# Optimization experiments

Hardware: AMD Instinct MI355X
Metric: run time of the kernel (lower is better)

The kernel has to match this reference:

```python
import jax, jax.numpy as jnp
import numpy as np

EPS = 1e-5

def _ln(x, g, b):
    mu = jnp.mean(x, axis=-1, keepdims=True)
    var = jnp.mean((x - mu) ** 2, axis=-1, keepdims=True)
    return (x - mu) * jax.lax.rsqrt(var + EPS) * g + b

def _leaky(x):
    return jax.nn.leaky_relu(x, 0.1)

def _gather(feats, idx):
    # feats: [B,N,C], idx: [B,M,K] -> [B,M,K,C]
    return jax.vmap(lambda f, i: f[i])(feats, idx)

def _forward(dense_xyz, dense_feats, pe_w1, pe_b1, pe_g1, pe_be1, pe_w2, pe_b2, pe_g2, pe_be2,
             wn_w1, wn_b1, wn_g1, wn_be1, wn_w2, wn_b2, wn_g2, wn_be2, wn_w3, wn_b3, wn_g3, wn_be3,
             nm_g, nm_b, l1_w, l1_b, l2_w, l2_b, sc_w, sc_b, nei_inds):
    gathered_xyz = _gather(dense_xyz, nei_inds)             # [B,M,K,3]
    localized = gathered_xyz - dense_xyz[:, :, None, :]     # relative coords (no subsampling: M==N)
    # pe_convs WeightNet: 3 -> 32 -> 32, LayerNorm per layer, LeakyReLU(0.1) except last
    h = _leaky(_ln(localized @ pe_w1 + pe_b1, pe_g1, pe_be1))
    feat_pe = _ln(h @ pe_w2 + pe_b2, pe_g2, pe_be2)         # [B,M,K,32]
    # weightnet: 3 -> 16 -> 16 -> Cin (per-edge depthwise weights)
    w = _leaky(_ln(localized @ wn_w1 + wn_b1, wn_g1, wn_be1))
    w = _leaky(_ln(w @ wn_w2 + wn_b2, wn_g2, wn_be2))
    w = _ln(w @ wn_w3 + wn_b3, wn_g3, wn_be3)               # [B,M,K,Cin]
    gathered_feat = _gather(dense_feats, nei_inds)          # [B,M,K,Cin]
    # depthwise aggregation over K, pe channels aggregated alongside
    agg = jnp.concatenate([jnp.sum(gathered_feat * w, axis=2), jnp.sum(feat_pe, axis=2)], axis=-1)
    x = _ln(agg, nm_g, nm_b)                                # LayerNorm(Cin+32)
    x = _leaky(x @ l1_w + l1_b)                             # inverted bottleneck 288 -> 1024
    x = x @ l2_w + l2_b                                     # 1024 -> Cout
    shortcut = dense_feats @ sc_w + sc_b                    # unary shortcut Cin -> Cout
    return _leaky(shortcut + x)

def setup_inputs():
    key = jax.random.key(0)
    B, N, K, CIN, COUT, PE, H = 1, 32768, 16, 256, 512, 32, 16
    ks = jax.random.split(key, 12)
    def g(k, shape, s=0.02):
        return jax.random.normal(k, shape, dtype=jnp.float32) * s
    return {
        "dense_xyz": jax.random.uniform(ks[0], (B, N, 3), dtype=jnp.float32),
        "dense_feats": jax.random.normal(ks[1], (B, N, CIN), dtype=jnp.float32),
        "nei_inds": jax.random.randint(ks[2], (B, N, K), 0, N),
        "pe_w1": g(ks[3], (3, PE), 0.2), "pe_b1": jnp.zeros((PE,), jnp.float32),
        "pe_g1": jnp.ones((PE,), jnp.float32), "pe_be1": jnp.zeros((PE,), jnp.float32),
        "pe_w2": g(ks[4], (PE, PE), 0.1), "pe_b2": jnp.zeros((PE,), jnp.float32),
        "pe_g2": jnp.ones((PE,), jnp.float32), "pe_be2": jnp.zeros((PE,), jnp.float32),
        "wn_w1": g(ks[5], (3, H), 0.2), "wn_b1": jnp.zeros((H,), jnp.float32),
        "wn_g1": jnp.ones((H,), jnp.float32), "wn_be1": jnp.zeros((H,), jnp.float32),
        "wn_w2": g(ks[6], (H, H), 0.1), "wn_b2": jnp.zeros((H,), jnp.float32),
        "wn_g2": jnp.ones((H,), jnp.float32), "wn_be2": jnp.zeros((H,), jnp.float32),
        "wn_w3": g(ks[7], (H, CIN), 0.1), "wn_b3": jnp.zeros((CIN,), jnp.float32),
        "wn_g3": jnp.ones((CIN,), jnp.float32), "wn_be3": jnp.zeros((CIN,), jnp.float32),
        "nm_g": jnp.ones((CIN + PE,), jnp.float32), "nm_b": jnp.zeros((CIN + PE,), jnp.float32),
        "l1_w": g(ks[8], (CIN + PE, 4 * CIN)), "l1_b": jnp.zeros((4 * CIN,), jnp.float32),
        "l2_w": g(ks[9], (4 * CIN, COUT)), "l2_b": jnp.zeros((COUT,), jnp.float32),
        "sc_w": g(ks[10], (CIN, COUT)), "sc_b": jnp.zeros((COUT,), jnp.float32),
    }

def reference(dense_xyz, dense_feats, nei_inds, pe_w1, pe_b1, pe_g1, pe_be1, pe_w2, pe_b2, pe_g2, pe_be2,
              wn_w1, wn_b1, wn_g1, wn_be1, wn_w2, wn_b2, wn_g2, wn_be2, wn_w3, wn_b3, wn_g3, wn_be3,
              nm_g, nm_b, l1_w, l1_b, l2_w, l2_b, sc_w, sc_b):
    return _forward(dense_xyz, dense_feats, pe_w1, pe_b1, pe_g1, pe_be1, pe_w2, pe_b2, pe_g2, pe_be2,
                    wn_w1, wn_b1, wn_g1, wn_be1, wn_w2, wn_b2, wn_g2, wn_be2, wn_w3, wn_b3, wn_g3, wn_be3,
                    nm_g, nm_b, l1_w, l1_b, l2_w, l2_b, sc_w, sc_b, nei_inds)
```

## Files before the change

### kernel.cpp

```cpp
#include <hip/hip_runtime.h>

#define NPTS  32768
#define KNB   16
#define CINC  256
#define PEC   32
#define HWN   16
#define CMID  288
#define L1OUT 1024
#define COUTC 512
#define EPSLN 1e-5f
#define PBLK  16

typedef __attribute__((ext_vector_type(8))) short short8;
typedef __attribute__((ext_vector_type(4))) float f32x4;

__device__ __forceinline__ float leaky(float x) { return x > 0.f ? x : 0.1f * x; }

__device__ __forceinline__ float bf2f(unsigned short u) {
    union { unsigned int i; float f; } x; x.i = ((unsigned int)u) << 16; return x.f;
}
__device__ __forceinline__ unsigned short f2bf(float f) {
    unsigned int x = __float_as_uint(f);
    x = (x + 0x7fffu + ((x >> 16) & 1u)) >> 16;
    return (unsigned short)x;
}

__device__ __forceinline__ void gld_lds16(const unsigned short* g, unsigned short* l) {
    __builtin_amdgcn_global_load_lds(
        (const __attribute__((address_space(1))) unsigned int*)g,
        (__attribute__((address_space(3))) unsigned int*)l,
        16, 0, 0);
}

__device__ __forceinline__ void stage_tile(const unsigned short* __restrict__ g,
                                           size_t ld, int row0, int k0,
                                           unsigned short* lds, int wave, int lane)
{
    #pragma unroll
    for (int r = 0; r < 2; ++r) {
        int e   = r * 2048 + wave * 512 + lane * 8;
        int row = e >> 5;
        int kp  = e & 31;
        int kl  = kp ^ ((row & 3) << 3);
        const unsigned short* src = g + (size_t)(row0 + row) * ld + (k0 + kl);
        gld_lds16(src, lds + r * 2048 + wave * 512);
    }
}

__global__ __launch_bounds__(256) void wn3_stats_kernel(
    const float* __restrict__ W3, const float* __restrict__ b3, float* __restrict__ st)
{
    const int b = blockIdx.x;
    const int t = threadIdx.x;
    const int lane = t & 63, wave = t >> 6;
    const int c0 = lane * 4;

    if (b < 64) {
        int pair = b * 4 + wave;
        int h = pair >> 4, hp = pair & 15;
        f32x4 a  = *(const f32x4*)(W3 + h * CINC + c0);
        f32x4 bb = *(const f32x4*)(W3 + hp * CINC + c0);
        float g = a[0] * bb[0] + a[1] * bb[1] + a[2] * bb[2] + a[3] * bb[3];
        #pragma unroll
        for (int off = 1; off < 64; off <<= 1) g += __shfl_xor(g, off);
        if (lane == 0) st[pair] = g * (1.f / CINC);
    } else if (b == 64) {
        #pragma unroll
        for (int i = 0; i < 4; ++i) {
            int h = wave * 4 + i;
            f32x4 w  = *(const f32x4*)(W3 + h * CINC + c0);
            f32x4 bb = *(const f32x4*)(b3 + c0);
            float s  = w[0] + w[1] + w[2] + w[3];
            float sb = w[0] * bb[0] + w[1] * bb[1] + w[2] * bb[2] + w[3] * bb[3];
            #pragma unroll
            for (int off = 1; off < 64; off <<= 1) { s += __shfl_xor(s, off); sb += __shfl_xor(sb, off); }
            if (lane == 0) { st[256 + h] = s * (1.f / CINC); st[272 + h] = sb * (1.f / CINC); }
        }
    } else if (wave == 0) {
        f32x4 bb = *(const f32x4*)(b3 + c0);
        float s = bb[0] + bb[1] + bb[2] + bb[3];
        float q = bb[0] * bb[0] + bb[1] * bb[1] + bb[2] * bb[2] + bb[3] * bb[3];
        #pragma unroll
        for (int off = 1; off < 64; off <<= 1) { s += __shfl_xor(s, off); q += __shfl_xor(q, off); }
        if (lane == 0) { st[288] = s * (1.f / CINC); st[289] = q * (1.f / CINC); }
    }
}

#define PEW1  0
#define PEB1  96
#define PEG1  128
#define PEBE1 160
#define PEW2  192
#define PEB2  1216
#define PEG2  1248
#define PEBE2 1280
#define WNW1  1312
#define WNB1  1360
#define WNG1  1376
#define WNBE1 1392
#define WNW2  1408
#define WNB2  1664
#define WNG2  1680
#define WNBE2 1696
#define STO   1712

__global__ __launch_bounds__(256, 3) void edge_fused_kernel(
    const float* __restrict__ xyz, const unsigned short* __restrict__ featsb,
    const int* __restrict__ nei,
    const float* __restrict__ pe_w1, const float* __restrict__ pe_b1,
    const float* __restrict__ pe_g1, const float* __restrict__ pe_be1,
    const float* __restrict__ pe_w2, const float* __restrict__ pe_b2,
    const float* __restrict__ pe_g2, const float* __restrict__ pe_be2,
    const float* __restrict__ wn_w1, const float* __restrict__ wn_b1,
    const float* __restrict__ wn_g1, const float* __restrict__ wn_be1,
    const float* __restrict__ wn_w2, const float* __restrict__ wn_b2,
    const float* __restrict__ wn_g2, const float* __restrict__ wn_be2,
    const float* __restrict__ st,
    const float* __restrict__ wn_w3, const float* __restrict__ wn_b3,
    const float* __restrict__ wn_g3, const float* __restrict__ wn_be3,
    const float* __restrict__ nm_g, const float* __restrict__ nm_b,
    unsigned short* __restrict__ xln)
{
    __shared__ __align__(16) float Ws[2008];
    __shared__ __align__(16) float W3s[16 * 256];
    __shared__ __align__(16) float w2s[PBLK * 256];
    __shared__ float rms[PBLK * 16], mus[PBLK * 16], pes[PBLK * 32];

    const int t = threadIdx.x;

    if (t < 96) Ws[PEW1 + t] = pe_w1[t];
    if (t < 32) {
        Ws[PEB1 + t] = pe_b1[t];  Ws[PEG1 + t] = pe_g1[t];  Ws[PEBE1 + t] = pe_be1[t];
        Ws[PEB2 + t] = pe_b2[t];  Ws[PEG2 + t] = pe_g2[t];  Ws[PEBE2 + t] = pe_be2[t];
    }
    for (int i = t; i < 1024; i += 256) Ws[PEW2 + i] = pe_w2[i];
    if (t < 48) Ws[WNW1 + t] = wn_w1[t];
    Ws[WNW2 + t] = wn_w2[t];
    if (t < 16) {
        Ws[WNB1 + t] = wn_b1[t];  Ws[WNG1 + t] = wn_g1[t];  Ws[WNBE1 + t] = wn_be1[t];
        Ws[WNB2 + t] = wn_b2[t];  Ws[WNG2 + t] = wn_g2[t];  Ws[WNBE2 + t] = wn_be2[t];
    }
    for (int i = t; i < 290; i += 256) Ws[STO + i] = st[i];
    for (int i = t; i < 4096; i += 256) W3s[i] = wn_w3[i];
    __syncthreads();

    {
        const int lp = t >> 4, kk = t & 15;
        const int m = blockIdx.x * PBLK + lp;
        const int n = nei[m * KNB + kk];
        const float lx = xyz[n * 3 + 0] - xyz[m * 3 + 0];
        const float ly = xyz[n * 3 + 1] - xyz[m * 3 + 1];
        const float lz = xyz[n * 3 + 2] - xyz[m * 3 + 2];

        float w1[16];
        float s = 0.f, q = 0.f;
        #pragma unroll
        for (int c4 = 0; c4 < 4; ++c4) {
            f32x4 wa = *(const f32x4*)&Ws[WNW1 + c4 * 4];
            f32x4 wb = *(const f32x4*)&Ws[WNW1 + 16 + c4 * 4];
            f32x4 wc = *(const f32x4*)&Ws[WNW1 + 32 + c4 * 4];
            f32x4 bb = *(const f32x4*)&Ws[WNB1 + c4 * 4];
            #pragma unroll
            for (int j = 0; j < 4; ++j) {
                float v = bb[j] + lx * wa[j] + ly * wb[j] + lz * wc[j];
                w1[c4 * 4 + j] = v; s += v; q += v * v;
            }
        }
        float mu = s * (1.f / 16.f);
        float rstd = rsqrtf(q * (1.f / 16.f) - mu * mu + EPSLN);
        #pragma unroll
        for (int c4 = 0; c4 < 4; ++c4) {
            f32x4 g = *(const f32x4*)&Ws[WNG1 + c4 * 4];
            f32x4 be = *(const f32x4*)&Ws[WNBE1 + c4 * 4];
            #pragma unroll
            for (int j = 0; j < 4; ++j) {
                int c = c4 * 4 + j;
                w1[c] = leaky((w1[c] - mu) * rstd * g[j] + be[j]);
            }
        }

        float w2[16];
        #pragma unroll
        for (int c4 = 0; c4 < 4; ++c4) {
            f32x4 bb = *(const f32x4*)&Ws[WNB2 + c4 * 4];
            w2[c4 * 4 + 0] = bb[0]; w2[c4 * 4 + 1] = bb[1];
            w2[c4 * 4 + 2] = bb[2]; w2[c4 * 4 + 3] = bb[3];
        }
        #pragma unroll 2
        for (int j = 0; j < 16; ++j) {
            float wj = w1[j];
            #pragma unroll
            for (int c4 = 0; c4 < 4; ++c4) {
                f32x4 w = *(const f32x4*)&Ws[WNW2 + j * 16 + c4 * 4];
                w2[c4 * 4 + 0] += wj * w[0]; w2[c4 * 4 + 1] += wj * w[1];
                w2[c4 * 4 + 2] += wj * w[2]; w2[c4 * 4 + 3] += wj * w[3];
            }
        }
        s = 0.f; q = 0.f;
        #pragma unroll
        for (int c = 0; c < 16; ++c) { s += w2[c]; q += w2[c] * w2[c]; }
        mu = s * (1.f / 16.f);
        rstd = rsqrtf(q * (1.f / 16.f) - mu * mu + EPSLN);
        #pragma unroll
        for (int c4 = 0; c4 < 4; ++c4) {
            f32x4 g = *(const f32x4*)&Ws[WNG2 + c4 * 4];
            f32x4 be = *(const f32x4*)&Ws[WNBE2 + c4 * 4];
            #pragma unroll
            for (int j = 0; j < 4; ++j) {
                int c = c4 * 4 + j;
                w2[c] = leaky((w2[c] - mu) * rstd * g[j] + be[j]);
            }
        }

        float mu3 = Ws[STO + 288];
        #pragma unroll
        for (int h4 = 0; h4 < 4; ++h4) {
            f32x4 wm = *(const f32x4*)&Ws[STO + 256 + h4 * 4];
            mu3 += w2[h4 * 4 + 0] * wm[0] + w2[h4 * 4 + 1] * wm[1]
                 + w2[h4 * 4 + 2] * wm[2] + w2[h4 * 4 + 3] * wm[3];
        }
        float esq = Ws[STO + 289];
        #pragma unroll 4
        for (int hh = 0; hh < 16; ++hh) {
            float acc = 2.f * Ws[STO + 272 + hh];
            #pragma unroll
            for (int h4 = 0; h4 < 4; ++h4) {
                f32x4 g = *(const f32x4*)&Ws[STO + hh * 16 + h4 * 4];
                acc += g[0] * w2[h4 * 4 + 0] + g[1] * w2[h4 * 4 + 1]
                     + g[2] * w2[h4 * 4 + 2] + g[3] * w2[h4 * 4 + 3];
            }
            esq += w2[hh] * acc;
        }
        float r3 = rsqrtf(esq - mu3 * mu3 + EPSLN);

        #pragma unroll
        for (int hh = 0; hh < 16; ++hh) w2s[lp * 256 + hh * 16 + kk] = w2[hh];
        rms[lp * 16 + kk] = r3;
        mus[lp * 16 + kk] = mu3;

        float h[32];
        s = 0.f; q = 0.f;
        #pragma unroll
        for (int c4 = 0; c4 < 8; ++c4) {
            f32x4 wa = *(const f32x4*)&Ws[PEW1 + c4 * 4];
            f32x4 wb = *(const f32x4*)&Ws[PEW1 + 32 + c4 * 4];
            f32x4 wc = *(const f32x4*)&Ws[PEW1 + 64 + c4 * 4];
            f32x4 bb = *(const f32x4*)&Ws[PEB1 + c4 * 4];
            #pragma unroll
            for (int j = 0; j < 4; ++j) {
                float v = bb[j] + lx * wa[j] + ly * wb[j] + lz * wc[j];
                h[c4 * 4 + j] = v; s += v; q += v * v;
            }
        }
        mu = s * (1.f / 32.f);
        rstd = rsqrtf(q * (1.f / 32.f) - mu * mu + EPSLN);
        #pragma unroll
        for (int c4 = 0; c4 < 8; ++c4) {
            f32x4 g = *(const f32x4*)&Ws[PEG1 + c4 * 4];
            f32x4 be = *(const f32x4*)&Ws[PEBE1 + c4 * 4];
            #pragma unroll
            for (int j = 0; j < 4; ++j) {
                int c = c4 * 4 + j;
                h[c] = leaky((h[c] - mu) * rstd * g[j] + be[j]);
            }
        }

        float f[32];
        #pragma unroll
        for (int c4 = 0; c4 < 8; ++c4) {
            f32x4 bb = *(const f32x4*)&Ws[PEB2 + c4 * 4];
            f[c4 * 4 + 0] = bb[0]; f[c4 * 4 + 1] = bb[1];
            f[c4 * 4 + 2] = bb[2]; f[c4 * 4 + 3] = bb[3];
        }
        #pragma unroll 2
        for (int j = 0; j < 32; ++j) {
            float hj = h[j];
            #pragma unroll
            for (int c4 = 0; c4 < 8; ++c4) {
                f32x4 w = *(const f32x4*)&Ws[PEW2 + j * 32 + c4 * 4];
                f[c4 * 4 + 0] += hj * w[0]; f[c4 * 4 + 1] += hj * w[1];
                f[c4 * 4 + 2] += hj * w[2]; f[c4 * 4 + 3] += hj * w[3];
            }
        }
        s = 0.f; q = 0.f;
        #pragma unroll
        for (int c = 0; c < 32; ++c) { s += f[c]; q += f[c] * f[c]; }
        mu = s * (1.f / 32.f);
        rstd = rsqrtf(q * (1.f / 32.f) - mu * mu + EPSLN);
        #pragma unroll
        for (int c4 = 0; c4 < 8; ++c4) {
            f32x4 g = *(const f32x4*)&Ws[PEG2 + c4 * 4];
            f32x4 be = *(const f32x4*)&Ws[PEBE2 + c4 * 4];
            #pragma unroll
            for (int j = 0; j < 4; ++j) {
                int c = c4 * 4 + j;
                float v = (f[c] - mu) * rstd * g[j] + be[j];
                v += __shfl_xor(v, 1);
                v += __shfl_xor(v, 2);
                v += __shfl_xor(v, 4);
                v += __shfl_xor(v, 8);
                if (kk == 0) pes[lp * 32 + c] = v;
            }
        }
    }
    __syncthreads();

    const int lane = t & 63, wave = t >> 6;
    const int c0 = lane * 4;
    const f32x4 b3r  = *(const f32x4*)(wn_b3 + c0);
    const f32x4 g3r  = *(const f32x4*)(wn_g3 + c0);
    const f32x4 be3r = *(const f32x4*)(wn_be3 + c0);

    for (int pp = 0; pp < 4; ++pp) {
        const int lp = wave * 4 + pp;
        const int p  = blockIdx.x * PBLK + lp;
        const int* np = nei + p * KNB;

        float agg[4] = {0.f, 0.f, 0.f, 0.f};

        #pragma unroll
        for (int kc = 0; kc < 2; ++kc) {
            float raw[8][4];
            #pragma unroll
            for (int k = 0; k < 8; ++k)
                #pragma unroll
                for (int j = 0; j < 4; ++j) raw[k][j] = 0.f;

            #pragma unroll 4
            for (int hh = 0; hh < 16; ++hh) {
                f32x4 w3r = *(const f32x4*)&W3s[hh * 256 + c0];
                f32x4 u0 = *(const f32x4*)&w2s[lp * 256 + hh * 16 + kc * 8];
                f32x4 u1 = *(const f32x4*)&w2s[lp * 256 + hh * 16 + kc * 8 + 4];
                #pragma unroll
                for (int k = 0; k < 4; ++k) {
                    raw[k][0] += u0[k] * w3r[0];
                    raw[k][1] += u0[k] * w3r[1];
                    raw[k][2] += u0[k] * w3r[2];
                    raw[k][3] += u0[k] * w3r[3];
                }
                #pragma unroll
                for (int k = 0; k < 4; ++k) {
                    raw[4 + k][0] += u1[k] * w3r[0];
                    raw[4 + k][1] += u1[k] * w3r[1];
                    raw[4 + k][2] += u1[k] * w3r[2];
                    raw[4 + k][3] += u1[k] * w3r[3];
                }
            }

            #pragma unroll
            for (int k8 = 0; k8 < 8; ++k8) {
                int k = kc * 8 + k8;
                int nk = np[k];
                float rk  = rms[lp * 16 + k];
                float muk = mus[lp * 16 + k];
                ushort4 fu = *(const ushort4*)(featsb + (size_t)nk * CINC + c0);
                float w3x = (raw[k8][0] + b3r[0] - muk) * rk * g3r[0] + be3r[0];
                float w3y = (raw[k8][1] + b3r[1] - muk) * rk * g3r[1] + be3r[1];
                float w3z = (raw[k8][2] + b3r[2] - muk) * rk * g3r[2] + be3r[2];
                float w3w = (raw[k8][3] + b3r[3] - muk) * rk * g3r[3] + be3r[3];
                agg[0] += bf2f(fu.x) * w3x;
                agg[1] += bf2f(fu.y) * w3y;
                agg[2] += bf2f(fu.z) * w3z;
                agg[3] += bf2f(fu.w) * w3w;
            }
        }

        float pv = (lane < 32) ? pes[lp * 32 + lane] : 0.f;

        float s = agg[0] + agg[1] + agg[2] + agg[3];
        float q = agg[0] * agg[0] + agg[1] * agg[1] + agg[2] * agg[2] + agg[3] * agg[3];
        if (lane < 32) { s += pv; q += pv * pv; }
        #pragma unroll
        for (int off = 1; off < 64; off <<= 1) {
            s += __shfl_xor(s, off);
            q += __shfl_xor(q, off);
        }
        float mu = s * (1.f / 288.f);
        float rstd = rsqrtf(q * (1.f / 288.f) - mu * mu + EPSLN);

        f32x4 ngr = *(const f32x4*)(nm_g + c0);
        f32x4 nbr = *(const f32x4*)(nm_b + c0);
        unsigned short* xp = xln + (size_t)p * CMID;
        ushort4 o;
        o.x = f2bf((agg[0] - mu) * rstd * ngr[0] + nbr[0]);
        o.y = f2bf((agg[1] - mu) * rstd * ngr[1] + nbr[1]);
        o.z = f2bf((agg[2] - mu) * rstd * ngr[2] + nbr[2]);
        o.w = f2bf((agg[3] - mu) * rstd * ngr[3] + nbr[3]);
        *(ushort4*)(xp + c0) = o;
        if (lane < 32)
            xp[256 + lane] = f2bf((pv - mu) * rstd * nm_g[256 + lane] + nm_b[256 + lane]);
    }
}

__global__ __launch_bounds__(256) void transpose_bf16_kernel(
    const float* __restrict__ src, unsigned short* __restrict__ dst, int K, int N)
{
    __shared__ float tile[32][33];
    const int k0 = blockIdx.y * 32, n0 = blockIdx.x * 32;
    const int tx = threadIdx.x & 31, ty = threadIdx.x >> 5;
    #pragma unroll
    for (int i = ty; i < 32; i += 8)
        tile[i][tx] = src[(size_t)(k0 + i) * N + n0 + tx];
    __syncthreads();
    #pragma unroll
    for (int i = ty; i < 32; i += 8)
        dst[(size_t)(n0 + i) * K + k0 + tx] = f2bf(tile[tx][i]);
}

__global__ __launch_bounds__(256) void feats_bf16_kernel(
    const float* __restrict__ src, unsigned short* __restrict__ dst)
{
    int i = (blockIdx.x * 256 + threadIdx.x) * 4;
    float4 v = *(const float4*)(src + i);
    ushort4 o;
    o.x = f2bf(v.x); o.y = f2bf(v.y); o.z = f2bf(v.z); o.w = f2bf(v.w);
    *(ushort4*)(dst + i) = o;
}

__global__ __launch_bounds__(256) void gemm1_mfma(
    const unsigned short* __restrict__ A,
    const unsigned short* __restrict__ BT,
    const float* __restrict__ bias,
    unsigned short* __restrict__ C)
{
    __shared__ unsigned short As[128 * 32];
    __shared__ unsigned short Bs[128 * 32];
    const int t = threadIdx.x;
    const int lane = t & 63, wave = t >> 6;
    const int wm = wave >> 1, wn = wave & 1;
    const int m0 = blockIdx.y * 128, n0 = blockIdx.x * 128;
    const int l15 = lane & 15, j0 = (lane >> 4) << 3;

    f32x4 zero = {0.f, 0.f, 0.f, 0.f};
    f32x4 acc[4][4];
    #pragma unroll
    for (int i = 0; i < 4; ++i)
        #pragma unroll
        for (int j = 0; j < 4; ++j) acc[i][j] = zero;

    for (int kt = 0; kt < CMID; kt += 32) {
        stage_tile(A,  CMID, m0, kt, As, wave, lane);
        stage_tile(BT, CMID, n0, kt, Bs, wave, lane);
        __syncthreads();
        short8 af[4], bf[4];
        #pragma unroll
        for (int i = 0; i < 4; ++i) {
            int ar = wm * 64 + i * 16 + l15;
            af[i] = *(const short8*)&As[ar * 32 + (j0 ^ ((ar & 3) << 3))];
            int br = wn * 64 + i * 16 + l15;
            bf[i] = *(const short8*)&Bs[br * 32 + (j0 ^ ((br & 3) << 3))];
        }
        #pragma unroll
        for (int i = 0; i < 4; ++i)
            #pragma unroll
            for (int j = 0; j < 4; ++j)
                acc[i][j] = __builtin_amdgcn_mfma_f32_16x16x32_bf16(af[i], bf[j], acc[i][j], 0, 0, 0);
        __syncthreads();
    }

    const int q = lane >> 4;
    #pragma unroll
    for (int j = 0; j < 4; ++j) {
        int ncol = n0 + wn * 64 + j * 16 + l15;
        float bv = bias[ncol];
        #pragma unroll
        for (int i = 0; i < 4; ++i) {
            int mbase = m0 + wm * 64 + i * 16 + q * 4;
            #pragma unroll
            for (int r = 0; r < 4; ++r)
                C[(size_t)(mbase + r) * L1OUT + ncol] = f2bf(leaky(acc[i][j][r] + bv));
        }
    }
}

__global__ __launch_bounds__(256) void gemm2_mfma(
    const unsigned short* __restrict__ H,
    const unsigned short* __restrict__ W2T,
    const unsigned short* __restrict__ F,
    const unsigned short* __restrict__ WscT,
    const float* __restrict__ b2, const float* __restrict__ bsc,
    float* __restrict__ Out)
{
    __shared__ unsigned short As[128 * 32];
    __shared__ unsigned short Bs[128 * 32];
    const int t = threadIdx.x;
    const int lane = t & 63, wave = t >> 6;
    const int wm = wave >> 1, wn = wave & 1;
    const int m0 = blockIdx.y * 128, n0 = blockIdx.x * 128;
    const int l15 = lane & 15, j0 = (lane >> 4) << 3;

    f32x4 zero = {0.f, 0.f, 0.f, 0.f};
    f32x4 acc[4][4];
    #pragma unroll
    for (int i = 0; i < 4; ++i)
        #pragma unroll
        for (int j = 0; j < 4; ++j) acc[i][j] = zero;

    for (int kt = 0; kt < L1OUT; kt += 32) {
        stage_tile(H,   L1OUT, m0, kt, As, wave, lane);
        stage_tile(W2T, L1OUT, n0, kt, Bs, wave, lane);
        __syncthreads();
        short8 af[4], bf[4];
        #pragma unroll
        for (int i = 0; i < 4; ++i) {
            int ar = wm * 64 + i * 16 + l15;
            af[i] = *(const short8*)&As[ar * 32 + (j0 ^ ((ar & 3) << 3))];
            int br = wn * 64 + i * 16 + l15;
            bf[i] = *(const short8*)&Bs[br * 32 + (j0 ^ ((br & 3) << 3))];
        }
        #pragma unroll
        for (int i = 0; i < 4; ++i)
            #pragma unroll
            for (int j = 0; j < 4; ++j)
                acc[i][j] = __builtin_amdgcn_mfma_f32_16x16x32_bf16(af[i], bf[j], acc[i][j], 0, 0, 0);
        __syncthreads();
    }
    for (int kt = 0; kt < CINC; kt += 32) {
        stage_tile(F,    CINC, m0, kt, As, wave, lane);
        stage_tile(WscT, CINC, n0, kt, Bs, wave, lane);
        __syncthreads();
        short8 af[4], bf[4];
        #pragma unroll
        for (int i = 0; i < 4; ++i) {
            int ar = wm * 64 + i * 16 + l15;
            af[i] = *(const short8*)&As[ar * 32 + (j0 ^ ((ar & 3) << 3))];
            int br = wn * 64 + i * 16 + l15;
            bf[i] = *(const short8*)&Bs[br * 32 + (j0 ^ ((br & 3) << 3))];
        }
        #pragma unroll
        for (int i = 0; i < 4; ++i)
            #pragma unroll
            for (int j = 0; j < 4; ++j)
                acc[i][j] = __builtin_amdgcn_mfma_f32_16x16x32_bf16(af[i], bf[j], acc[i][j], 0, 0, 0);
        __syncthreads();
    }

    const int q = lane >> 4;
    #pragma unroll
    for (int j = 0; j < 4; ++j) {
        int ncol = n0 + wn * 64 + j * 16 + l15;
        float bv = b2[ncol] + bsc[ncol];
        #pragma unroll
        for (int i = 0; i < 4; ++i) {
            int mbase = m0 + wm * 64 + i * 16 + q * 4;
            #pragma unroll
            for (int r = 0; r < 4; ++r)
                Out[(size_t)(mbase + r) * COUTC + ncol] = leaky(acc[i][j][r] + bv);
        }
    }
}

extern "C" void kernel_launch(void* const* d_in, const int* in_sizes, int n_in,
                              void* d_out, int out_size, void* d_ws, size_t ws_size,
                              hipStream_t stream)
{
    const float* xyz    = (const float*)d_in[0];
    const float* feats  = (const float*)d_in[1];
    const int*   nei    = (const int*)d_in[2];
    const float* pe_w1  = (const float*)d_in[3];
    const float* pe_b1  = (const float*)d_in[4];
    const float* pe_g1  = (const float*)d_in[5];
    const float* pe_be1 = (const float*)d_in[6];
    const float* pe_w2  = (const float*)d_in[7];
    const float* pe_b2  = (const float*)d_in[8];
    const float* pe_g2  = (const float*)d_in[9];
    const float* pe_be2 = (const float*)d_in[10];
    const float* wn_w1  = (const float*)d_in[11];
    const float* wn_b1  = (const float*)d_in[12];
    const float* wn_g1  = (const float*)d_in[13];
    const float* wn_be1 = (const float*)d_in[14];
    const float* wn_w2  = (const float*)d_in[15];
    const float* wn_b2  = (const float*)d_in[16];
    const float* wn_g2  = (const float*)d_in[17];
    const float* wn_be2 = (const float*)d_in[18];
    const float* wn_w3  = (const float*)d_in[19];
    const float* wn_b3  = (const float*)d_in[20];
    const float* wn_g3  = (const float*)d_in[21];
    const float* wn_be3 = (const float*)d_in[22];
    const float* nm_g   = (const float*)d_in[23];
    const float* nm_b   = (const float*)d_in[24];
    const float* l1_w   = (const float*)d_in[25];
    const float* l1_b   = (const float*)d_in[26];
    const float* l2_w   = (const float*)d_in[27];
    const float* l2_b   = (const float*)d_in[28];
    const float* sc_w   = (const float*)d_in[29];
    const float* sc_b   = (const float*)d_in[30];

    char* ws = (char*)d_ws;
    unsigned short* xln    = (unsigned short*)(ws);
    unsigned short* featsb = (unsigned short*)(ws + 18874368);
    unsigned short* l1_wT  = (unsigned short*)(ws + 35651584);
    unsigned short* l2_wT  = (unsigned short*)(ws + 36241408);
    unsigned short* sc_wT  = (unsigned short*)(ws + 37289984);
    float*          st     = (float*)(ws + 37552128);
    unsigned short* h1     = (unsigned short*)(ws + 37556224);

    wn3_stats_kernel<<<66, 256, 0, stream>>>(wn_w3, wn_b3, st);
    transpose_bf16_kernel<<<dim3(L1OUT / 32, CMID / 32), 256, 0, stream>>>(l1_w, l1_wT, CMID, L1OUT);
    transpose_bf16_kernel<<<dim3(COUTC / 32, L1OUT / 32), 256, 0, stream>>>(l2_w, l2_wT, L1OUT, COUTC);
    transpose_bf16_kernel<<<dim3(COUTC / 32, CINC / 32), 256, 0, stream>>>(sc_w, sc_wT, CINC, COUTC);
    feats_bf16_kernel<<<(NPTS * CINC / 4) / 256, 256, 0, stream>>>(feats, featsb);

    edge_fused_kernel<<<NPTS / PBLK, 256, 0, stream>>>(
        xyz, featsb, nei,
        pe_w1, pe_b1, pe_g1, pe_be1, pe_w2, pe_b2, pe_g2, pe_be2,
        wn_w1, wn_b1, wn_g1, wn_be1, wn_w2, wn_b2, wn_g2, wn_be2,
        st, wn_w3, wn_b3, wn_g3, wn_be3, nm_g, nm_b, xln);

    gemm1_mfma<<<dim3(L1OUT / 128, NPTS / 128), 256, 0, stream>>>(xln, l1_wT, l1_b, h1);

    gemm2_mfma<<<dim3(COUTC / 128, NPTS / 128), 256, 0, stream>>>(
        h1, l2_wT, featsb, sc_wT, l2_b, sc_b, (float*)d_out);
}
```

Measured before the change: 416.4 us.

## Drop LDS weight staging, async-load W3 to LDS, raise occupancy in edge kernel

The small MLP weights are no longer copied into a shared Ws array; they are read directly from global memory with uniform addresses, which lets the compiler use scalar loads and frees LDS. The W3 weight tile is staged with global_load_lds direct-to-LDS copies, and the explicit barrier after staging is removed. The launch bound is raised from 3 to 4 blocks per CU. The two half-K raw accumulation passes are merged into one 16-neighbour pass with vectorised reads of the rms/mu statistics. The merged pass holds 64 accumulators per thread under a tighter register budget, which risks spills. The barrier removal also relies on a later barrier and a memory-count wait to make the W3 tile visible before it is used.

```diff
diff --git a/kernel.cpp b/kernel.cpp
--- a/kernel.cpp
+++ b/kernel.cpp
@@ -31,6 +31,12 @@
         (__attribute__((address_space(3))) unsigned int*)l,
         16, 0, 0);
 }
+__device__ __forceinline__ void gld_lds16f(const float* g, float* l) {
+    __builtin_amdgcn_global_load_lds(
+        (const __attribute__((address_space(1))) unsigned int*)g,
+        (__attribute__((address_space(3))) unsigned int*)l,
+        16, 0, 0);
+}
 
 __device__ __forceinline__ void stage_tile(const unsigned short* __restrict__ g,
                                            size_t ld, int row0, int k0,
@@ -86,25 +92,7 @@
     }
 }
 
-#define PEW1  0
-#define PEB1  96
-#define PEG1  128
-#define PEBE1 160
-#define PEW2  192
-#define PEB2  1216
-#define PEG2  1248
-#define PEBE2 1280
-#define WNW1  1312
-#define WNB1  1360
-#define WNG1  1376
-#define WNBE1 1392
-#define WNW2  1408
-#define WNB2  1664
-#define WNG2  1680
-#define WNBE2 1696
-#define STO   1712
-
-__global__ __launch_bounds__(256, 3) void edge_fused_kernel(
+__global__ __launch_bounds__(256, 4) void edge_fused_kernel(
     const float* __restrict__ xyz, const unsigned short* __restrict__ featsb,
     const int* __restrict__ nei,
     const float* __restrict__ pe_w1, const float* __restrict__ pe_b1,
@@ -121,28 +109,21 @@
     const float* __restrict__ nm_g, const float* __restrict__ nm_b,
     unsigned short* __restrict__ xln)
 {
-    __shared__ __align__(16) float Ws[2008];
     __shared__ __align__(16) float W3s[16 * 256];
     __shared__ __align__(16) float w2s[PBLK * 256];
-    __shared__ float rms[PBLK * 16], mus[PBLK * 16], pes[PBLK * 32];
+    __shared__ float rms[PBLK * 16], mus[PBLK * 16];
+    __shared__ float pes[PBLK * 32];
 
     const int t = threadIdx.x;
 
-    if (t < 96) Ws[PEW1 + t] = pe_w1[t];
-    if (t < 32) {
-        Ws[PEB1 + t] = pe_b1[t];  Ws[PEG1 + t] = pe_g1[t];  Ws[PEBE1 + t] = pe_be1[t];
-        Ws[PEB2 + t] = pe_b2[t];  Ws[PEG2 + t] = pe_g2[t];  Ws[PEBE2 + t] = pe_be2[t];
-    }
-    for (int i = t; i < 1024; i += 256) Ws[PEW2 + i] = pe_w2[i];
-    if (t < 48) Ws[WNW1 + t] = wn_w1[t];
-    Ws[WNW2 + t] = wn_w2[t];
-    if (t < 16) {
-        Ws[WNB1 + t] = wn_b1[t];  Ws[WNG1 + t] = wn_g1[t];  Ws[WNBE1 + t] = wn_be1[t];
-        Ws[WNB2 + t] = wn_b2[t];  Ws[WNG2 + t] = wn_g2[t];  Ws[WNBE2 + t] = wn_be2[t];
-    }
-    for (int i = t; i < 290; i += 256) Ws[STO + i] = st[i];
-    for (int i = t; i < 4096; i += 256) W3s[i] = wn_w3[i];
-    __syncthreads();
+    {
+        const int lane = t & 63, wave = t >> 6;
+        #pragma unroll
+        for (int r = 0; r < 4; ++r) {
+            int base = (wave * 4 + r) * 256;
+            gld_lds16f(wn_w3 + base + lane * 4, W3s + base);
+        }
+    }
 
     {
         const int lp = t >> 4, kk = t & 15;
@@ -156,10 +137,10 @@
         float s = 0.f, q = 0.f;
         #pragma unroll
         for (int c4 = 0; c4 < 4; ++c4) {
-            f32x4 wa = *(const f32x4*)&Ws[WNW1 + c4 * 4];
-            f32x4 wb = *(const f32x4*)&Ws[WNW1 + 16 + c4 * 4];
-            f32x4 wc = *(const f32x4*)&Ws[WNW1 + 32 + c4 * 4];
-            f32x4 bb = *(const f32x4*)&Ws[WNB1 + c4 * 4];
+            f32x4 wa = *(const f32x4*)&wn_w1[c4 * 4];
+            f32x4 wb = *(const f32x4*)&wn_w1[16 + c4 * 4];
+            f32x4 wc = *(const f32x4*)&wn_w1[32 + c4 * 4];
+            f32x4 bb = *(const f32x4*)&wn_b1[c4 * 4];
             #pragma unroll
             for (int j = 0; j < 4; ++j) {
                 float v = bb[j] + lx * wa[j] + ly * wb[j] + lz * wc[j];
@@ -170,8 +151,8 @@
         float rstd = rsqrtf(q * (1.f / 16.f) - mu * mu + EPSLN);
         #pragma unroll
         for (int c4 = 0; c4 < 4; ++c4) {
-            f32x4 g = *(const f32x4*)&Ws[WNG1 + c4 * 4];
-            f32x4 be = *(const f32x4*)&Ws[WNBE1 + c4 * 4];
+            f32x4 g = *(const f32x4*)&wn_g1[c4 * 4];
+            f32x4 be = *(const f32x4*)&wn_be1[c4 * 4];
             #pragma unroll
             for (int j = 0; j < 4; ++j) {
                 int c = c4 * 4 + j;
@@ -182,7 +163,7 @@
         float w2[16];
         #pragma unroll
         for (int c4 = 0; c4 < 4; ++c4) {
-            f32x4 bb = *(const f32x4*)&Ws[WNB2 + c4 * 4];
+            f32x4 bb = *(const f32x4*)&wn_b2[c4 * 4];
             w2[c4 * 4 + 0] = bb[0]; w2[c4 * 4 + 1] = bb[1];
             w2[c4 * 4 + 2] = bb[2]; w2[c4 * 4 + 3] = bb[3];
         }
@@ -191,7 +172,7 @@
             float wj = w1[j];
             #pragma unroll
             for (int c4 = 0; c4 < 4; ++c4) {
-                f32x4 w = *(const f32x4*)&Ws[WNW2 + j * 16 + c4 * 4];
+                f32x4 w = *(const f32x4*)&wn_w2[j * 16 + c4 * 4];
                 w2[c4 * 4 + 0] += wj * w[0]; w2[c4 * 4 + 1] += wj * w[1];
                 w2[c4 * 4 + 2] += wj * w[2]; w2[c4 * 4 + 3] += wj * w[3];
             }
@@ -203,8 +184,8 @@
         rstd = rsqrtf(q * (1.f / 16.f) - mu * mu + EPSLN);
         #pragma unroll
         for (int c4 = 0; c4 < 4; ++c4) {
-            f32x4 g = *(const f32x4*)&Ws[WNG2 + c4 * 4];
-            f32x4 be = *(const f32x4*)&Ws[WNBE2 + c4 * 4];
+            f32x4 g = *(const f32x4*)&wn_g2[c4 * 4];
+            f32x4 be = *(const f32x4*)&wn_be2[c4 * 4];
             #pragma unroll
             for (int j = 0; j < 4; ++j) {
                 int c = c4 * 4 + j;
@@ -212,20 +193,20 @@
             }
         }
 
-        float mu3 = Ws[STO + 288];
+        float mu3 = st[288];
         #pragma unroll
         for (int h4 = 0; h4 < 4; ++h4) {
-            f32x4 wm = *(const f32x4*)&Ws[STO + 256 + h4 * 4];
+            f32x4 wm = *(const f32x4*)&st[256 + h4 * 4];
             mu3 += w2[h4 * 4 + 0] * wm[0] + w2[h4 * 4 + 1] * wm[1]
                  + w2[h4 * 4 + 2] * wm[2] + w2[h4 * 4 + 3] * wm[3];
         }
-        float esq = Ws[STO + 289];
+        float esq = st[289];
         #pragma unroll 4
         for (int hh = 0; hh < 16; ++hh) {
-            float acc = 2.f * Ws[STO + 272 + hh];
+            float acc = 2.f * st[272 + hh];
             #pragma unroll
             for (int h4 = 0; h4 < 4; ++h4) {
-                f32x4 g = *(const f32x4*)&Ws[STO + hh * 16 + h4 * 4];
+                f32x4 g = *(const f32x4*)&st[hh * 16 + h4 * 4];
                 acc += g[0] * w2[h4 * 4 + 0] + g[1] * w2[h4 * 4 + 1]
                      + g[2] * w2[h4 * 4 + 2] + g[3] * w2[h4 * 4 + 3];
             }
@@ -242,10 +223,10 @@
         s = 0.f; q = 0.f;
         #pragma unroll
         for (int c4 = 0; c4 < 8; ++c4) {
-            f32x4 wa = *(const f32x4*)&Ws[PEW1 + c4 * 4];
-            f32x4 wb = *(const f32x4*)&Ws[PEW1 + 32 + c4 * 4];
-            f32x4 wc = *(const f32x4*)&Ws[PEW1 + 64 + c4 * 4];
-            f32x4 bb = *(const f32x4*)&Ws[PEB1 + c4 * 4];
+            f32x4 wa = *(const f32x4*)&pe_w1[c4 * 4];
+            f32x4 wb = *(const f32x4*)&pe_w1[32 + c4 * 4];
+            f32x4 wc = *(const f32x4*)&pe_w1[64 + c4 * 4];
+            f32x4 bb = *(const f32x4*)&pe_b1[c4 * 4];
             #pragma unroll
             for (int j = 0; j < 4; ++j) {
                 float v = bb[j] + lx * wa[j] + ly * wb[j] + lz * wc[j];
@@ -256,8 +237,8 @@
         rstd = rsqrtf(q * (1.f / 32.f) - mu * mu + EPSLN);
         #pragma unroll
         for (int c4 = 0; c4 < 8; ++c4) {
-            f32x4 g = *(const f32x4*)&Ws[PEG1 + c4 * 4];
-            f32x4 be = *(const f32x4*)&Ws[PEBE1 + c4 * 4];
+            f32x4 g = *(const f32x4*)&pe_g1[c4 * 4];
+            f32x4 be = *(const f32x4*)&pe_be1[c4 * 4];
             #pragma unroll
             for (int j = 0; j < 4; ++j) {
                 int c = c4 * 4 + j;
@@ -268,7 +249,7 @@
         float f[32];
         #pragma unroll
         for (int c4 = 0; c4 < 8; ++c4) {
-            f32x4 bb = *(const f32x4*)&Ws[PEB2 + c4 * 4];
+            f32x4 bb = *(const f32x4*)&pe_b2[c4 * 4];
             f[c4 * 4 + 0] = bb[0]; f[c4 * 4 + 1] = bb[1];
             f[c4 * 4 + 2] = bb[2]; f[c4 * 4 + 3] = bb[3];
         }
@@ -277,7 +258,7 @@
             float hj = h[j];
             #pragma unroll
             for (int c4 = 0; c4 < 8; ++c4) {
-                f32x4 w = *(const f32x4*)&Ws[PEW2 + j * 32 + c4 * 4];
+                f32x4 w = *(const f32x4*)&pe_w2[j * 32 + c4 * 4];
                 f[c4 * 4 + 0] += hj * w[0]; f[c4 * 4 + 1] += hj * w[1];
                 f[c4 * 4 + 2] += hj * w[2]; f[c4 * 4 + 3] += hj * w[3];
             }
@@ -289,8 +270,8 @@
         rstd = rsqrtf(q * (1.f / 32.f) - mu * mu + EPSLN);
         #pragma unroll
         for (int c4 = 0; c4 < 8; ++c4) {
-            f32x4 g = *(const f32x4*)&Ws[PEG2 + c4 * 4];
-            f32x4 be = *(const f32x4*)&Ws[PEBE2 + c4 * 4];
+            f32x4 g = *(const f32x4*)&pe_g2[c4 * 4];
+            f32x4 be = *(const f32x4*)&pe_be2[c4 * 4];
             #pragma unroll
             for (int j = 0; j < 4; ++j) {
                 int c = c4 * 4 + j;
@@ -316,48 +297,65 @@
         const int p  = blockIdx.x * PBLK + lp;
         const int* np = nei + p * KNB;
 
+        float raw[16][4];
+        #pragma unroll
+        for (int k = 0; k < 16; ++k)
+            #pragma unroll
+            for (int j = 0; j < 4; ++j) raw[k][j] = 0.f;
+
+        #pragma unroll 4
+        for (int hh = 0; hh < 16; ++hh) {
+            f32x4 w3r = *(const f32x4*)&W3s[hh * 256 + c0];
+            f32x4 u0 = *(const f32x4*)&w2s[lp * 256 + hh * 16 + 0];
+            f32x4 u1 = *(const f32x4*)&w2s[lp * 256 + hh * 16 + 4];
+            f32x4 u2 = *(const f32x4*)&w2s[lp * 256 + hh * 16 + 8];
+            f32x4 u3 = *(const f32x4*)&w2s[lp * 256 + hh * 16 + 12];
+            #pragma unroll
+            for (int k = 0; k < 4; ++k) {
+                raw[k][0] += u0[k] * w3r[0];
+                raw[k][1] += u0[k] * w3r[1];
+                raw[k][2] += u0[k] * w3r[2];
+                raw[k][3] += u0[k] * w3r[3];
+            }
+            #pragma unroll
+            for (int k = 0; k < 4; ++k) {
+                raw[4 + k][0] += u1[k] * w3r[0];
+                raw[4 + k][1] += u1[k] * w3r[1];
+                raw[4 + k][2] += u1[k] * w3r[2];
+                raw[4 + k][3] += u1[k] * w3r[3];
+            }
+            #pragma unroll
+            for (int k = 0; k < 4; ++k) {
+                raw[8 + k][0] += u2[k] * w3r[0];
+                raw[8 + k][1] += u2[k] * w3r[1];
+                raw[8 + k][2] += u2[k] * w3r[2];
+                raw[8 + k][3] += u2[k] * w3r[3];
+            }
+            #pragma unroll
+            for (int k = 0; k < 4; ++k) {
+                raw[12 + k][0] += u3[k] * w3r[0];
+                raw[12 + k][1] += u3[k] * w3r[1];
+                raw[12 + k][2] += u3[k] * w3r[2];
+                raw[12 + k][3] += u3[k] * w3r[3];
+            }
+        }
+
         float agg[4] = {0.f, 0.f, 0.f, 0.f};
-
-        #pragma unroll
-        for (int kc = 0; kc < 2; ++kc) {
-            float raw[8][4];
-            #pragma unroll
-            for (int k = 0; k < 8; ++k)
-                #pragma unroll
-                for (int j = 0; j < 4; ++j) raw[k][j] = 0.f;
-
-            #pragma unroll 4
-            for (int hh = 0; hh < 16; ++hh) {
-                f32x4 w3r = *(const f32x4*)&W3s[hh * 256 + c0];
-                f32x4 u0 = *(const f32x4*)&w2s[lp * 256 + hh * 16 + kc * 8];
-                f32x4 u1 = *(const f32x4*)&w2s[lp * 256 + hh * 16 + kc * 8 + 4];
-                #pragma unroll
-                for (int k = 0; k < 4; ++k) {
-                    raw[k][0] += u0[k] * w3r[0];
-                    raw[k][1] += u0[k] * w3r[1];
-                    raw[k][2] += u0[k] * w3r[2];
-                    raw[k][3] += u0[k] * w3r[3];
-                }
-                #pragma unroll
-                for (int k = 0; k < 4; ++k) {
-                    raw[4 + k][0] += u1[k] * w3r[0];
-                    raw[4 + k][1] += u1[k] * w3r[1];
-                    raw[4 + k][2] += u1[k] * w3r[2];
-                    raw[4 + k][3] += u1[k] * w3r[3];
-                }
-            }
-
-            #pragma unroll
-            for (int k8 = 0; k8 < 8; ++k8) {
-                int k = kc * 8 + k8;
+        #pragma unroll
+        for (int k4 = 0; k4 < 4; ++k4) {
+            f32x4 rkv = *(const f32x4*)&rms[lp * 16 + k4 * 4];
+            f32x4 muv = *(const f32x4*)&mus[lp * 16 + k4 * 4];
+            #pragma unroll
+            for (int r = 0; r < 4; ++r) {
+                int k = k4 * 4 + r;
                 int nk = np[k];
-                float rk  = rms[lp * 16 + k];
-                float muk = mus[lp * 16 + k];
+                float rk  = rkv[r];
+                float muk = muv[r];
                 ushort4 fu = *(const ushort4*)(featsb + (size_t)nk * CINC + c0);
-                float w3x = (raw[k8][0] + b3r[0] - muk) * rk * g3r[0] + be3r[0];
-                float w3y = (raw[k8][1] + b3r[1] - muk) * rk * g3r[1] + be3r[1];
-                float w3z = (raw[k8][2] + b3r[2] - muk) * rk * g3r[2] + be3r[2];
-                float w3w = (raw[k8][3] + b3r[3] - muk) * rk * g3r[3] + be3r[3];
+                float w3x = (raw[k][0] + b3r[0] - muk) * rk * g3r[0] + be3r[0];
+                float w3y = (raw[k][1] + b3r[1] - muk) * rk * g3r[1] + be3r[1];
+                float w3z = (raw[k][2] + b3r[2] - muk) * rk * g3r[2] + be3r[2];
+                float w3w = (raw[k][3] + b3r[3] - muk) * rk * g3r[3] + be3r[3];
                 agg[0] += bf2f(fu.x) * w3x;
                 agg[1] += bf2f(fu.y) * w3y;
                 agg[2] += bf2f(fu.z) * w3z;
```

After: 540.2 us. 29.7% more time.

## Use packed FP32 FMA in edge kernel and read W3 from global

Applied to the files above, without the earlier changes.

Rewrites the per-edge weightnet and PE MLP inner products and the W3 expansion loop to use v_pk_fma_f32 via inline asm, processing two channels per instruction. It removes the 16 KB W3 shared-memory tile, reading wn_w3 directly from global/cache instead, which shrinks LDS use per block and may allow more resident blocks. The w2s buffer gets a padded stride to reduce bank conflicts, and rms/mus are read as vectors. Risks include extra global/L2 traffic for W3 and inline-asm constraints limiting compiler scheduling; the kc loop is no longer fully unrolled.

```diff
diff --git a/kernel.cpp b/kernel.cpp
--- a/kernel.cpp
+++ b/kernel.cpp
@@ -10,9 +10,11 @@
 #define COUTC 512
 #define EPSLN 1e-5f
 #define PBLK  16
+#define W2LD  272
 
 typedef __attribute__((ext_vector_type(8))) short short8;
 typedef __attribute__((ext_vector_type(4))) float f32x4;
+typedef __attribute__((ext_vector_type(2))) float f32x2;
 
 __device__ __forceinline__ float leaky(float x) { return x > 0.f ? x : 0.1f * x; }
 
@@ -23,6 +25,19 @@
     unsigned int x = __float_as_uint(f);
     x = (x + 0x7fffu + ((x >> 16) & 1u)) >> 16;
     return (unsigned short)x;
+}
+
+__device__ __forceinline__ f32x2 lo2(f32x4 v) { return __builtin_shufflevector(v, v, 0, 1); }
+__device__ __forceinline__ f32x2 hi2(f32x4 v) { return __builtin_shufflevector(v, v, 2, 3); }
+
+__device__ __forceinline__ void pkfma(f32x2& d, f32x2 a, f32x2 b) {
+    asm("v_pk_fma_f32 %0, %1, %2, %0" : "+v"(d) : "v"(a), "v"(b));
+}
+__device__ __forceinline__ void pkfma_lo(f32x2& d, f32x2 a, f32x2 b) {
+    asm("v_pk_fma_f32 %0, %1, %2, %0 op_sel:[0,0,0] op_sel_hi:[0,1,1]" : "+v"(d) : "v"(a), "v"(b));
+}
+__device__ __forceinline__ void pkfma_hi(f32x2& d, f32x2 a, f32x2 b) {
+    asm("v_pk_fma_f32 %0, %1, %2, %0 op_sel:[1,0,0] op_sel_hi:[1,1,1]" : "+v"(d) : "v"(a), "v"(b));
 }
 
 __device__ __forceinline__ void gld_lds16(const unsigned short* g, unsigned short* l) {
@@ -122,9 +137,10 @@
     unsigned short* __restrict__ xln)
 {
     __shared__ __align__(16) float Ws[2008];
-    __shared__ __align__(16) float W3s[16 * 256];
-    __shared__ __align__(16) float w2s[PBLK * 256];
-    __shared__ float rms[PBLK * 16], mus[PBLK * 16], pes[PBLK * 32];
+    __shared__ __align__(16) float w2s[PBLK * W2LD];
+    __shared__ __align__(16) float rms[PBLK * 16];
+    __shared__ __align__(16) float mus[PBLK * 16];
+    __shared__ float pes[PBLK * 32];
 
     const int t = threadIdx.x;
 
@@ -141,7 +157,6 @@
         Ws[WNB2 + t] = wn_b2[t];  Ws[WNG2 + t] = wn_g2[t];  Ws[WNBE2 + t] = wn_be2[t];
     }
     for (int i = t; i < 290; i += 256) Ws[STO + i] = st[i];
-    for (int i = t; i < 4096; i += 256) W3s[i] = wn_w3[i];
     __syncthreads();
 
     {
@@ -152,7 +167,7 @@
         const float ly = xyz[n * 3 + 1] - xyz[m * 3 + 1];
         const float lz = xyz[n * 3 + 2] - xyz[m * 3 + 2];
 
-        float w1[16];
+        f32x2 w1p[8];
         float s = 0.f, q = 0.f;
         #pragma unroll
         for (int c4 = 0; c4 < 4; ++c4) {
@@ -163,7 +178,8 @@
             #pragma unroll
             for (int j = 0; j < 4; ++j) {
                 float v = bb[j] + lx * wa[j] + ly * wb[j] + lz * wc[j];
-                w1[c4 * 4 + j] = v; s += v; q += v * v;
+                int c = c4 * 4 + j;
+                w1p[c >> 1][c & 1] = v; s += v; q += v * v;
             }
         }
         float mu = s * (1.f / 16.f);
@@ -175,30 +191,38 @@
             #pragma unroll
             for (int j = 0; j < 4; ++j) {
                 int c = c4 * 4 + j;
-                w1[c] = leaky((w1[c] - mu) * rstd * g[j] + be[j]);
-            }
-        }
-
-        float w2[16];
+                w1p[c >> 1][c & 1] = leaky((w1p[c >> 1][c & 1] - mu) * rstd * g[j] + be[j]);
+            }
+        }
+
+        f32x2 w2p[8];
         #pragma unroll
         for (int c4 = 0; c4 < 4; ++c4) {
             f32x4 bb = *(const f32x4*)&Ws[WNB2 + c4 * 4];
-            w2[c4 * 4 + 0] = bb[0]; w2[c4 * 4 + 1] = bb[1];
-            w2[c4 * 4 + 2] = bb[2]; w2[c4 * 4 + 3] = bb[3];
+            w2p[c4 * 2] = lo2(bb); w2p[c4 * 2 + 1] = hi2(bb);
         }
         #pragma unroll 2
-        for (int j = 0; j < 16; ++j) {
-            float wj = w1[j];
+        for (int jp = 0; jp < 8; ++jp) {
+            f32x2 hp = w1p[jp];
             #pragma unroll
             for (int c4 = 0; c4 < 4; ++c4) {
-                f32x4 w = *(const f32x4*)&Ws[WNW2 + j * 16 + c4 * 4];
-                w2[c4 * 4 + 0] += wj * w[0]; w2[c4 * 4 + 1] += wj * w[1];
-                w2[c4 * 4 + 2] += wj * w[2]; w2[c4 * 4 + 3] += wj * w[3];
+                f32x4 w = *(const f32x4*)&Ws[WNW2 + (2 * jp) * 16 + c4 * 4];
+                pkfma_lo(w2p[c4 * 2], hp, lo2(w));
+                pkfma_lo(w2p[c4 * 2 + 1], hp, hi2(w));
+            }
+            #pragma unroll
+            for (int c4 = 0; c4 < 4; ++c4) {
+                f32x4 w = *(const f32x4*)&Ws[WNW2 + (2 * jp + 1) * 16 + c4 * 4];
+                pkfma_hi(w2p[c4 * 2], hp, lo2(w));
+                pkfma_hi(w2p[c4 * 2 + 1], hp, hi2(w));
             }
         }
         s = 0.f; q = 0.f;
         #pragma unroll
-        for (int c = 0; c < 16; ++c) { s += w2[c]; q += w2[c] * w2[c]; }
+        for (int i = 0; i < 8; ++i) {
+            s += w2p[i][0] + w2p[i][1];
+            q += w2p[i][0] * w2p[i][0] + w2p[i][1] * w2p[i][1];
+        }
         mu = s * (1.f / 16.f);
         rstd = rsqrtf(q * (1.f / 16.f) - mu * mu + EPSLN);
         #pragma unroll
@@ -208,7 +232,7 @@
             #pragma unroll
             for (int j = 0; j < 4; ++j) {
                 int c = c4 * 4 + j;
-                w2[c] = leaky((w2[c] - mu) * rstd * g[j] + be[j]);
+                w2p[c >> 1][c & 1] = leaky((w2p[c >> 1][c & 1] - mu) * rstd * g[j] + be[j]);
             }
         }
 
@@ -216,29 +240,31 @@
         #pragma unroll
         for (int h4 = 0; h4 < 4; ++h4) {
             f32x4 wm = *(const f32x4*)&Ws[STO + 256 + h4 * 4];
-            mu3 += w2[h4 * 4 + 0] * wm[0] + w2[h4 * 4 + 1] * wm[1]
-                 + w2[h4 * 4 + 2] * wm[2] + w2[h4 * 4 + 3] * wm[3];
+            mu3 += wm[0] * w2p[h4 * 2][0] + wm[1] * w2p[h4 * 2][1]
+                 + wm[2] * w2p[h4 * 2 + 1][0] + wm[3] * w2p[h4 * 2 + 1][1];
         }
         float esq = Ws[STO + 289];
         #pragma unroll 4
         for (int hh = 0; hh < 16; ++hh) {
-            float acc = 2.f * Ws[STO + 272 + hh];
+            f32x2 acc2 = {0.f, 0.f};
             #pragma unroll
             for (int h4 = 0; h4 < 4; ++h4) {
                 f32x4 g = *(const f32x4*)&Ws[STO + hh * 16 + h4 * 4];
-                acc += g[0] * w2[h4 * 4 + 0] + g[1] * w2[h4 * 4 + 1]
-                     + g[2] * w2[h4 * 4 + 2] + g[3] * w2[h4 * 4 + 3];
-            }
-            esq += w2[hh] * acc;
+                pkfma(acc2, lo2(g), w2p[h4 * 2]);
+                pkfma(acc2, hi2(g), w2p[h4 * 2 + 1]);
+            }
+            float acc = acc2[0] + acc2[1] + 2.f * Ws[STO + 272 + hh];
+            esq += w2p[hh >> 1][hh & 1] * acc;
         }
         float r3 = rsqrtf(esq - mu3 * mu3 + EPSLN);
 
         #pragma unroll
-        for (int hh = 0; hh < 16; ++hh) w2s[lp * 256 + hh * 16 + kk] = w2[hh];
+        for (int hh = 0; hh < 16; ++hh)
+            w2s[lp * W2LD + hh * 16 + kk] = w2p[hh >> 1][hh & 1];
         rms[lp * 16 + kk] = r3;
         mus[lp * 16 + kk] = mu3;
 
-        float h[32];
+        f32x2 h2[16];
         s = 0.f; q = 0.f;
         #pragma unroll
         for (int c4 = 0; c4 < 8; ++c4) {
@@ -249,7 +275,8 @@
             #pragma unroll
             for (int j = 0; j < 4; ++j) {
                 float v = bb[j] + lx * wa[j] + ly * wb[j] + lz * wc[j];
-                h[c4 * 4 + j] = v; s += v; q += v * v;
+                int c = c4 * 4 + j;
+                h2[c >> 1][c & 1] = v; s += v; q += v * v;
             }
         }
         mu = s * (1.f / 32.f);
@@ -261,30 +288,38 @@
             #pragma unroll
             for (int j = 0; j < 4; ++j) {
                 int c = c4 * 4 + j;
-                h[c] = leaky((h[c] - mu) * rstd * g[j] + be[j]);
-            }
-        }
-
-        float f[32];
+                h2[c >> 1][c & 1] = leaky((h2[c >> 1][c & 1] - mu) * rstd * g[j] + be[j]);
+            }
+        }
+
+        f32x2 f2[16];
         #pragma unroll
         for (int c4 = 0; c4 < 8; ++c4) {
             f32x4 bb = *(const f32x4*)&Ws[PEB2 + c4 * 4];
-            f[c4 * 4 + 0] = bb[0]; f[c4 * 4 + 1] = bb[1];
-            f[c4 * 4 + 2] = bb[2]; f[c4 * 4 + 3] = bb[3];
+            f2[c4 * 2] = lo2(bb); f2[c4 * 2 + 1] = hi2(bb);
         }
         #pragma unroll 2
-        for (int j = 0; j < 32; ++j) {
-            float hj = h[j];
+        for (int jp = 0; jp < 16; ++jp) {
+            f32x2 hp = h2[jp];
             #pragma unroll
             for (int c4 = 0; c4 < 8; ++c4) {
-                f32x4 w = *(const f32x4*)&Ws[PEW2 + j * 32 + c4 * 4];
-                f[c4 * 4 + 0] += hj * w[0]; f[c4 * 4 + 1] += hj * w[1];
-                f[c4 * 4 + 2] += hj * w[2]; f[c4 * 4 + 3] += hj * w[3];
+                f32x4 w = *(const f32x4*)&Ws[PEW2 + (2 * jp) * 32 + c4 * 4];
+                pkfma_lo(f2[c4 * 2], hp, lo2(w));
+                pkfma_lo(f2[c4 * 2 + 1], hp, hi2(w));
+            }
+            #pragma unroll
+            for (int c4 = 0; c4 < 8; ++c4) {
+                f32x4 w = *(const f32x4*)&Ws[PEW2 + (2 * jp + 1) * 32 + c4 * 4];
+                pkfma_hi(f2[c4 * 2], hp, lo2(w));
+                pkfma_hi(f2[c4 * 2 + 1], hp, hi2(w));
             }
         }
         s = 0.f; q = 0.f;
         #pragma unroll
-        for (int c = 0; c < 32; ++c) { s += f[c]; q += f[c] * f[c]; }
+        for (int i = 0; i < 16; ++i) {
+            s += f2[i][0] + f2[i][1];
+            q += f2[i][0] * f2[i][0] + f2[i][1] * f2[i][1];
+        }
         mu = s * (1.f / 32.f);
         rstd = rsqrtf(q * (1.f / 32.f) - mu * mu + EPSLN);
         #pragma unroll
@@ -294,7 +329,7 @@
             #pragma unroll
             for (int j = 0; j < 4; ++j) {
                 int c = c4 * 4 + j;
-                float v = (f[c] - mu) * rstd * g[j] + be[j];
+                float v = (f2[c >> 1][c & 1] - mu) * rstd * g[j] + be[j];
                 v += __shfl_xor(v, 1);
                 v += __shfl_xor(v, 2);
                 v += __shfl_xor(v, 4);
@@ -318,46 +353,63 @@
 
         float agg[4] = {0.f, 0.f, 0.f, 0.f};
 
-        #pragma unroll
         for (int kc = 0; kc < 2; ++kc) {
-            float raw[8][4];
-            #pragma unroll
-            for (int k = 0; k < 8; ++k)
-                #pragma unroll
-                for (int j = 0; j < 4; ++j) raw[k][j] = 0.f;
+            f32x2 raw2[8][2];
+            #pragma unroll
+            for (int k = 0; k < 8; ++k) {
+                raw2[k][0] = (f32x2){0.f, 0.f};
+                raw2[k][1] = (f32x2){0.f, 0.f};
+            }
 
             #pragma unroll 4
             for (int hh = 0; hh < 16; ++hh) {
-                f32x4 w3r = *(const f32x4*)&W3s[hh * 256 + c0];
-                f32x4 u0 = *(const f32x4*)&w2s[lp * 256 + hh * 16 + kc * 8];
-                f32x4 u1 = *(const f32x4*)&w2s[lp * 256 + hh * 16 + kc * 8 + 4];
-                #pragma unroll
-                for (int k = 0; k < 4; ++k) {
-                    raw[k][0] += u0[k] * w3r[0];
-                    raw[k][1] += u0[k] * w3r[1];
-                    raw[k][2] += u0[k] * w3r[2];
-                    raw[k][3] += u0[k] * w3r[3];
-                }
-                #pragma unroll
-                for (int k = 0; k < 4; ++k) {
-                    raw[4 + k][0] += u1[k] * w3r[0];
-                    raw[4 + k][1] += u1[k] * w3r[1];
-                    raw[4 + k][2] += u1[k] * w3r[2];
-                    raw[4 + k][3] += u1[k] * w3r[3];
-                }
-            }
-
-            #pragma unroll
-            for (int k8 = 0; k8 < 8; ++k8) {
-                int k = kc * 8 + k8;
+                f32x4 w3r = *(const f32x4*)&wn_w3[hh * 256 + c0];
+                f32x2 w01 = lo2(w3r), w23 = hi2(w3r);
+                f32x4 u0 = *(const f32x4*)&w2s[lp * W2LD + hh * 16 + kc * 8];
+                f32x4 u1 = *(const f32x4*)&w2s[lp * W2LD + hh * 16 + kc * 8 + 4];
+                f32x2 p0 = lo2(u0), p1 = hi2(u0), p2 = lo2(u1), p3 = hi2(u1);
+                pkfma_lo(raw2[0][0], p0, w01); pkfma_lo(raw2[0][1], p0, w23);
+                pkfma_hi(raw2[1][0], p0, w01); pkfma_hi(raw2[1][1], p0, w23);
+                pkfma_lo(raw2[2][0], p1, w01); pkfma_lo(raw2[2][1], p1, w23);
+                pkfma_hi(raw2[3][0], p1, w01); pkfma_hi(raw2[3][1], p1, w23);
+                pkfma_lo(raw2[4][0], p2, w01); pkfma_lo(raw2[4][1], p2, w23);
+                pkfma_hi(raw2[5][0], p2, w01); pkfma_hi(raw2[5][1], p2, w23);
+                pkfma_lo(raw2[6][0], p3, w01); pkfma_lo(raw2[6][1], p3, w23);
+                pkfma_hi(raw2[7][0], p3, w01); pkfma_hi(raw2[7][1], p3, w23);
+            }
+
+            f32x4 rkv = *(const f32x4*)&rms[lp * 16 + kc * 8];
+            f32x4 rk2 = *(const f32x4*)&rms[lp * 16 + kc * 8 + 4];
+            f32x4 muv = *(const f32x4*)&mus[lp * 16 + kc * 8];
+            f32x4 mu2 = *(const f32x4*)&mus[lp * 16 + kc * 8 + 4];
+
+            #pragma unroll
+            for (int r = 0; r < 4; ++r) {
+                int k = kc * 8 + r;
                 int nk = np[k];
-                float rk  = rms[lp * 16 + k];
-                float muk = mus[lp * 16 + k];
+                float rk  = rkv[r];
+                float muk = muv[r];
                 ushort4 fu = *(const ushort4*)(featsb + (size_t)nk * CINC + c0);
-                float w3x = (raw[k8][0] + b3r[0] - muk) * rk * g3r[0] + be3r[0];
-                float w3y = (raw[k8][1] + b3r[1] - muk) * rk * g3r[1] + be3r[1];
-                float w3z = (raw[k8][2] + b3r[2] - muk) * rk * g3r[2] + be3r[2];
-                float w3w = (raw[k8][3] + b3r[3] - muk) * rk * g3r[3] + be3r[3];
+                float w3x = (raw2[r][0][0] + b3r[0] - muk) * rk * g3r[0] + be3r[0];
+                float w3y = (raw2[r][0][1] + b3r[1] - muk) * rk * g3r[1] + be3r[1];
+                float w3z = (raw2[r][1][0] + b3r[2] - muk) * rk * g3r[2] + be3r[2];
+                float w3w = (raw2[r][1][1] + b3r[3] - muk) * rk * g3r[3] + be3r[3];
+                agg[0] += bf2f(fu.x) * w3x;
+                agg[1] += bf2f(fu.y) * w3y;
+                agg[2] += bf2f(fu.z) * w3z;
+                agg[3] += bf2f(fu.w) * w3w;
+            }
+            #pragma unroll
+            for (int r = 0; r < 4; ++r) {
+                int k = kc * 8 + 4 + r;
+                int nk = np[k];
+                float rk  = rk2[r];
+                float muk = mu2[r];
+                ushort4 fu = *(const ushort4*)(featsb + (size_t)nk * CINC + c0);
+                float w3x = (raw2[4 + r][0][0] + b3r[0] - muk) * rk * g3r[0] + be3r[0];
+                float w3y = (raw2[4 + r][0][1] + b3r[1] - muk) * rk * g3r[1] + be3r[1];
+                float w3z = (raw2[4 + r][1][0] + b3r[2] - muk) * rk * g3r[2] + be3r[2];
+                float w3w = (raw2[4 + r][1][1] + b3r[3] - muk) * rk * g3r[3] + be3r[3];
                 agg[0] += bf2f(fu.x) * w3x;
                 agg[1] += bf2f(fu.y) * w3y;
                 agg[2] += bf2f(fu.z) * w3z;
```

New measurement: 438.1 us. 1.05x slower.
